# Optimization experiments

Measured on AMD Instinct MI355X. Metric: run time of the kernel, lower is better.

Reference implementation:

```python
import jax, jax.numpy as jnp
import numpy as np

T, B = 1024, 512
IN_F, HID, OUT = 64, 128, 2
DT = 0.001

# SuperSpike surrogate gradient (norse default threshold method='super')
@jax.custom_vjp
def superspike(x, alpha):
    return (x > 0).astype(x.dtype)

def _ss_fwd(x, alpha):
    return superspike(x, alpha), (x, alpha)

def _ss_bwd(res, g):
    x, alpha = res
    return (g / (alpha * jnp.abs(x) + 1.0) ** 2, jnp.zeros_like(alpha))

superspike.defvjp(_ss_fwd, _ss_bwd)


def setup_inputs() -> dict:
    key = jax.random.key(0)
    ks = jax.random.split(key, 6)
    x = jax.random.normal(ks[0], (T, B, IN_F), jnp.float32)
    # nn.Linear(input, hidden, bias=False)
    W_in = jax.random.normal(ks[1], (HID, IN_F), jnp.float32) / np.sqrt(IN_F)
    # LIFRecurrentCell(hidden, hidden) weights (norse init scale sqrt(2/hidden))
    cell_W_in = jax.random.normal(ks[2], (HID, HID), jnp.float32) * np.sqrt(2.0 / HID)
    cell_W_rec = jax.random.normal(ks[3], (HID, HID), jnp.float32) * np.sqrt(2.0 / HID)
    cell_W_rec = cell_W_rec * (1.0 - jnp.eye(HID, dtype=jnp.float32))  # autapses=False
    # nn.Linear(hidden, output, bias=True)
    W_out = jax.random.normal(ks[4], (OUT, HID), jnp.float32) / np.sqrt(HID)
    b_out = jax.random.normal(ks[5], (OUT,), jnp.float32) * 0.01
    # LIFParameters as in __init__
    alpha = jnp.full((HID,), 100.0, jnp.float32)
    v_th = jnp.full((HID,), 1.0, jnp.float32)
    v_leak = jnp.asarray(0.0, jnp.float32)
    v_reset = jnp.full((HID,), 0.0, jnp.float32)
    tau_mem_inv = jnp.full((HID,), 100.0, jnp.float32)
    tau_syn_inv = jnp.full((HID,), 200.0, jnp.float32)
    return dict(x=x, W_in=W_in, cell_W_in=cell_W_in, cell_W_rec=cell_W_rec,
                W_out=W_out, b_out=b_out, alpha=alpha, v_th=v_th, v_leak=v_leak,
                v_reset=v_reset, tau_mem_inv=tau_mem_inv, tau_syn_inv=tau_syn_inv)


def reference(x, W_in, cell_W_in, cell_W_rec, W_out, b_out,
              alpha, v_th, v_leak, v_reset, tau_mem_inv, tau_syn_inv):
    Tn, Bn, _ = x.shape
    H = W_in.shape[0]

    def step(carry, x_t):
        z, v, i = carry                                   # each [B,H]
        inp = x_t @ W_in.T                                # input_layer
        # norse _lif_step: decay v and i, spike, reset, inject currents
        v_dec = v + DT * tau_mem_inv * ((v_leak - v) + i)
        i_dec = i - DT * tau_syn_inv * i
        z_new = superspike(v_dec - v_th, alpha)
        v_new = (1.0 - z_new) * v_dec + z_new * v_reset
        i_new = i_dec + inp @ cell_W_in.T + z @ cell_W_rec.T
        out_t = z_new @ W_out.T + b_out                   # output_layer
        return (z_new, v_new, i_new), (out_t, jnp.sum(z_new))

    init = (jnp.zeros((Bn, H), x.dtype),
            jnp.zeros((Bn, H), x.dtype),
            jnp.zeros((Bn, H), x.dtype))
    _, (outs, spk) = jax.lax.scan(step, init, x)
    z_sum = jnp.sum(outs, axis=0)                         # __decode_sum over time
    spikerate = jnp.sum(spk) / (Tn * Bn * H)
    return z_sum, spikerate
```

## Files before the change

kernel.cpp:

```cpp
#include <hip/hip_runtime.h>
#include <stdint.h>

#define T_STEPS 1024
#define BATCH   512
#define INF     64
#define HID     128
#define OUTF    2

__global__ void zero_kernel(unsigned int* __restrict__ counter)
{
    *counter = 0u;
}

#define FOR16(M) M(0)M(1)M(2)M(3)M(4)M(5)M(6)M(7)M(8)M(9)M(10)M(11)M(12)M(13)M(14)M(15)
#define FOR32(M) FOR16(M) M(16)M(17)M(18)M(19)M(20)M(21)M(22)M(23)M(24)M(25)M(26)M(27)M(28)M(29)M(30)M(31)

#define BARRIER() asm volatile("s_waitcnt lgkmcnt(0)\n\ts_barrier" ::: "memory")

__global__ __launch_bounds__(256) __attribute__((amdgpu_waves_per_eu(2, 2)))
void snn_seq(const float* __restrict__ x,
             const float* __restrict__ W_in,
             const float* __restrict__ cWi,
             const float* __restrict__ Wrec,
             const float* __restrict__ W_out,
             const float* __restrict__ b_out,
             const float* __restrict__ v_th,
             const float* __restrict__ v_leak1,
             const float* __restrict__ v_reset,
             const float* __restrict__ tau_mem,
             const float* __restrict__ tau_syn,
             float* __restrict__ out,
             unsigned int* __restrict__ counter)
{
    #pragma clang fp contract(off)

    extern __shared__ char smem[];
    float* Wrec_T  = (float*)smem;
    float* x_lds   = Wrec_T + HID * HID;
    float* inp_lds = x_lds + 2 * INF;
    float* pre_lds = inp_lds + 2 * HID;

    const int tid = threadIdx.x;
    const int b   = blockIdx.x;

    for (int idx = tid; idx < HID * HID; idx += 256)
        Wrec_T[idx] = Wrec[(idx & (HID - 1)) * HID + (idx >> 7)];
    if (tid >= 128 && tid < 192) {
        int l = tid - 128;
        x_lds[0 * INF + l] = x[(size_t)(0 * BATCH + b) * INF + l];
        x_lds[1 * INF + l] = x[(size_t)(1 * BATCH + b) * INF + l];
    }
    __syncthreads();

    if (tid < 128) {
        const int h = tid;
        const float4* cwr = (const float4*)(cWi + h * HID);
        #define DECL_C(q) float4 c##q = cwr[q];
        FOR32(DECL_C)
        #undef DECL_C

        BARRIER();

        {
            const float4* ir4 = (const float4*)(inp_lds + 0 * HID);
            float p = 0.f;
            #define S2(q) { float4 i4 = ir4[q]; \
                p = fmaf(i4.x, c##q.x, p); p = fmaf(i4.y, c##q.y, p); \
                p = fmaf(i4.z, c##q.z, p); p = fmaf(i4.w, c##q.w, p); }
            FOR32(S2)
            pre_lds[0 * HID + h] = p;
            BARRIER();

            for (int i = 0; i < T_STEPS; ++i) {
                const int nbuf = (i & 1) ^ 1;
                const float4* ir = (const float4*)(inp_lds + nbuf * HID);
                float pp = 0.f;
                #undef S2
                #define S2(q) { float4 i4 = ir[q]; \
                    pp = fmaf(i4.x, c##q.x, pp); pp = fmaf(i4.y, c##q.y, pp); \
                    pp = fmaf(i4.z, c##q.z, pp); pp = fmaf(i4.w, c##q.w, pp); }
                FOR32(S2)
                #undef S2
                pre_lds[nbuf * HID + h] = pp;
                BARRIER();
            }
        }
    } else if (tid < 192) {
        const int l = tid - 128;
        const float4* wra = (const float4*)(W_in + l * INF);
        const float4* wrb = (const float4*)(W_in + (l + 64) * INF);
        #define DECL_AB(q) float4 a##q = wra[q]; float4 b##q = wrb[q];
        FOR16(DECL_AB)
        #undef DECL_AB

        #define S1(q) { float4 x4 = xr4[q]; \
            sa = fmaf(x4.x, a##q.x, sa); sa = fmaf(x4.y, a##q.y, sa); \
            sa = fmaf(x4.z, a##q.z, sa); sa = fmaf(x4.w, a##q.w, sa); \
            sb = fmaf(x4.x, b##q.x, sb); sb = fmaf(x4.y, b##q.y, sb); \
            sb = fmaf(x4.z, b##q.z, sb); sb = fmaf(x4.w, b##q.w, sb); }

        {
            const float4* xr4 = (const float4*)(x_lds + 0 * INF);
            float sa = 0.f, sb = 0.f;
            FOR16(S1)
            inp_lds[0 * HID + l] = sa;
            inp_lds[0 * HID + 64 + l] = sb;
        }
        BARRIER();

        float xnext;
        {
            const float4* xr4 = (const float4*)(x_lds + 1 * INF);
            float sa = 0.f, sb = 0.f;
            FOR16(S1)
            inp_lds[1 * HID + l] = sa;
            inp_lds[1 * HID + 64 + l] = sb;
            x_lds[0 * INF + l] = x[(size_t)(2 * BATCH + b) * INF + l];
            xnext = x[(size_t)(3 * BATCH + b) * INF + l];
        }
        BARRIER();

        for (int i = 0; i < T_STEPS; ++i) {
            const int buf  = i & 1;
            const int nbuf = buf ^ 1;
            x_lds[nbuf * INF + l] = xnext;
            int tn = (i + 4 < T_STEPS) ? i + 4 : T_STEPS - 1;
            xnext = x[((size_t)tn * BATCH + b) * INF + l];
            const float4* xr4 = (const float4*)(x_lds + buf * INF);
            float sa = 0.f, sb = 0.f;
            FOR16(S1)
            inp_lds[buf * HID + l] = sa;
            inp_lds[buf * HID + 64 + l] = sb;
            BARRIER();
        }
        #undef S1
    } else {
        const int l  = tid - 192;
        const int h0 = 2 * l, h1 = 2 * l + 1;

        const double vth0  = (double)v_th[h0],    vth1  = (double)v_th[h1];
        const double vleak = (double)v_leak1[0];
        const double vrs0  = (double)v_reset[h0], vrs1  = (double)v_reset[h1];
        const double dtm0  = 0.001 * (double)tau_mem[h0];
        const double dtm1  = 0.001 * (double)tau_mem[h1];
        const double dts0  = 0.001 * (double)tau_syn[h0];
        const double dts1  = 0.001 * (double)tau_syn[h1];

        double v0 = 0.0, v1 = 0.0, c0 = 0.0, c1 = 0.0;
        int cnt0 = 0, cnt1 = 0;
        unsigned long long me = 0ull, mo = 0ull;

        BARRIER();
        BARRIER();

        for (int i = 0; i < T_STEPS; ++i) {
            const int buf = i & 1;
            float2 pp = *(const float2*)(pre_lds + buf * HID + h0);

            double s00 = 0.0, s01 = 0.0, s10 = 0.0, s11 = 0.0;
            {
                unsigned long long A = me, Bm = mo;
                while (A | Bm) {
                    float2 w0 = make_float2(0.f, 0.f), w1 = w0, w2 = w0, w3 = w0,
                           w4 = w0, w5 = w0, w6 = w0, w7 = w0;
                    if (A)  { int j = __builtin_ctzll(A);  A  &= A - 1;  w0 = *(const float2*)(Wrec_T + (2 * j) * HID + h0); }
                    if (A)  { int j = __builtin_ctzll(A);  A  &= A - 1;  w1 = *(const float2*)(Wrec_T + (2 * j) * HID + h0); }
                    if (A)  { int j = __builtin_ctzll(A);  A  &= A - 1;  w2 = *(const float2*)(Wrec_T + (2 * j) * HID + h0); }
                    if (A)  { int j = __builtin_ctzll(A);  A  &= A - 1;  w3 = *(const float2*)(Wrec_T + (2 * j) * HID + h0); }
                    if (Bm) { int j = __builtin_ctzll(Bm); Bm &= Bm - 1; w4 = *(const float2*)(Wrec_T + (2 * j + 1) * HID + h0); }
                    if (Bm) { int j = __builtin_ctzll(Bm); Bm &= Bm - 1; w5 = *(const float2*)(Wrec_T + (2 * j + 1) * HID + h0); }
                    if (Bm) { int j = __builtin_ctzll(Bm); Bm &= Bm - 1; w6 = *(const float2*)(Wrec_T + (2 * j + 1) * HID + h0); }
                    if (Bm) { int j = __builtin_ctzll(Bm); Bm &= Bm - 1; w7 = *(const float2*)(Wrec_T + (2 * j + 1) * HID + h0); }
                    s00 += (double)w0.x; s10 += (double)w0.y;
                    s01 += (double)w1.x; s11 += (double)w1.y;
                    s00 += (double)w2.x; s10 += (double)w2.y;
                    s01 += (double)w3.x; s11 += (double)w3.y;
                    s00 += (double)w4.x; s10 += (double)w4.y;
                    s01 += (double)w5.x; s11 += (double)w5.y;
                    s00 += (double)w6.x; s10 += (double)w6.y;
                    s01 += (double)w7.x; s11 += (double)w7.y;
                }
            }
            double rec0 = s00 + s01;
            double rec1 = s10 + s11;

            double vd0 = v0 + dtm0 * ((vleak - v0) + c0);
            double id0 = c0 - dts0 * c0;
            bool   z0  = (vd0 - vth0) > 0.0;
            v0 = z0 ? vrs0 : vd0;
            c0 = (id0 + (double)pp.x) + rec0;
            cnt0 += z0 ? 1 : 0;

            double vd1 = v1 + dtm1 * ((vleak - v1) + c1);
            double id1 = c1 - dts1 * c1;
            bool   z1  = (vd1 - vth1) > 0.0;
            v1 = z1 ? vrs1 : vd1;
            c1 = (id1 + (double)pp.y) + rec1;
            cnt1 += z1 ? 1 : 0;

            me = __ballot(z0);
            mo = __ballot(z1);
            BARRIER();
        }

        pre_lds[h0] = (float)cnt0;
        pre_lds[h1] = (float)cnt1;
    }

    __syncthreads();

    const float* cnt_lds = pre_lds;
    if (tid < OUTF) {
        double sAcc = 0.0;
        for (int hh = 0; hh < HID; ++hh)
            sAcc += (double)cnt_lds[hh] * (double)W_out[tid * HID + hh];
        out[(size_t)b * OUTF + tid] = (float)(sAcc + 1024.0 * (double)b_out[tid]);
    }
    if (tid == 0) {
        unsigned int tot = 0;
        for (int k2 = 0; k2 < HID; ++k2) tot += (unsigned int)cnt_lds[k2];
        atomicAdd(counter, tot);
    }
}

__global__ void finalize_kernel(float* __restrict__ out)
{
    unsigned int c = ((const unsigned int*)out)[BATCH * OUTF];
    out[BATCH * OUTF] = (float)c * 0x1p-26f;
}

extern "C" void kernel_launch(void* const* d_in, const int* in_sizes, int n_in,
                              void* d_out, int out_size, void* d_ws, size_t ws_size,
                              hipStream_t stream) {
    (void)in_sizes; (void)n_in; (void)d_ws; (void)ws_size; (void)out_size;

    const float* x       = (const float*)d_in[0];
    const float* W_in    = (const float*)d_in[1];
    const float* cWi     = (const float*)d_in[2];
    const float* cWr     = (const float*)d_in[3];
    const float* W_out   = (const float*)d_in[4];
    const float* b_out   = (const float*)d_in[5];
    const float* v_th    = (const float*)d_in[7];
    const float* v_leak  = (const float*)d_in[8];
    const float* v_reset = (const float*)d_in[9];
    const float* tau_mem = (const float*)d_in[10];
    const float* tau_syn = (const float*)d_in[11];
    float* out = (float*)d_out;
    unsigned int* counter = (unsigned int*)out + BATCH * OUTF;

    zero_kernel<<<1, 1, 0, stream>>>(counter);

    const size_t lds_bytes =
        (size_t)(HID * HID + 2 * INF + 2 * HID + 2 * HID) * sizeof(float);
    snn_seq<<<dim3(512), dim3(256), lds_bytes, stream>>>(
        x, W_in, cWi, cWr, W_out, b_out, v_th, v_leak, v_reset,
        tau_mem, tau_syn, out, counter);

    finalize_kernel<<<1, 1, 0, stream>>>(out);
}
```

Before: 733.6 us.

## Deepen warp-specialized pipeline to 8 waves with split matvec stages

Doubles the block to 512 threads and splits the per-step work into more pipeline stages. The cell input matvec is split across two wavefronts that each hold half the weights. The input projection now uses 128 threads, each computing one output. A dedicated wavefront prefetches x into a 4-slot ring. The aim is to shorten each stage's critical path so the barrier-synchronised step loop runs faster, at the cost of more waves, more barriers in flight and extra pipeline latency.

```diff
diff --git a/kernel.cpp b/kernel.cpp
--- a/kernel.cpp
+++ b/kernel.cpp
@@ -13,11 +13,9 @@
 }
 
 #define FOR16(M) M(0)M(1)M(2)M(3)M(4)M(5)M(6)M(7)M(8)M(9)M(10)M(11)M(12)M(13)M(14)M(15)
-#define FOR32(M) FOR16(M) M(16)M(17)M(18)M(19)M(20)M(21)M(22)M(23)M(24)M(25)M(26)M(27)M(28)M(29)M(30)M(31)
-
 #define BARRIER() asm volatile("s_waitcnt lgkmcnt(0)\n\ts_barrier" ::: "memory")
 
-__global__ __launch_bounds__(256) __attribute__((amdgpu_waves_per_eu(2, 2)))
+__global__ __launch_bounds__(512, 4)
 void snn_seq(const float* __restrict__ x,
              const float* __restrict__ W_in,
              const float* __restrict__ cWi,
@@ -36,106 +34,144 @@
 
     extern __shared__ char smem[];
     float* Wrec_T  = (float*)smem;
-    float* x_lds   = Wrec_T + HID * HID;
-    float* inp_lds = x_lds + 2 * INF;
-    float* pre_lds = inp_lds + 2 * HID;
+    float* inp_lds = Wrec_T + HID * HID;
+    float* x_lds   = inp_lds + 4 * HID;
+    float* q_lds   = x_lds + 4 * INF;
+    float* pre_lds = q_lds + 2 * HID;
 
     const int tid = threadIdx.x;
     const int b   = blockIdx.x;
 
-    for (int idx = tid; idx < HID * HID; idx += 256)
+    for (int idx = tid; idx < HID * HID; idx += 512)
         Wrec_T[idx] = Wrec[(idx & (HID - 1)) * HID + (idx >> 7)];
-    if (tid >= 128 && tid < 192) {
-        int l = tid - 128;
-        x_lds[0 * INF + l] = x[(size_t)(0 * BATCH + b) * INF + l];
-        x_lds[1 * INF + l] = x[(size_t)(1 * BATCH + b) * INF + l];
-    }
-    __syncthreads();
 
     if (tid < 128) {
         const int h = tid;
         const float4* cwr = (const float4*)(cWi + h * HID);
         #define DECL_C(q) float4 c##q = cwr[q];
-        FOR32(DECL_C)
+        FOR16(DECL_C)
         #undef DECL_C
 
-        BARRIER();
-
+        #define S2A(q) { float4 i4 = ir4[q]; \
+            acc = fmaf(i4.x, c##q.x, acc); acc = fmaf(i4.y, c##q.y, acc); \
+            acc = fmaf(i4.z, c##q.z, acc); acc = fmaf(i4.w, c##q.w, acc); }
+
+        __syncthreads();
+        BARRIER();
         {
             const float4* ir4 = (const float4*)(inp_lds + 0 * HID);
-            float p = 0.f;
-            #define S2(q) { float4 i4 = ir4[q]; \
-                p = fmaf(i4.x, c##q.x, p); p = fmaf(i4.y, c##q.y, p); \
-                p = fmaf(i4.z, c##q.z, p); p = fmaf(i4.w, c##q.w, p); }
-            FOR32(S2)
-            pre_lds[0 * HID + h] = p;
-            BARRIER();
-
-            for (int i = 0; i < T_STEPS; ++i) {
-                const int nbuf = (i & 1) ^ 1;
-                const float4* ir = (const float4*)(inp_lds + nbuf * HID);
-                float pp = 0.f;
-                #undef S2
-                #define S2(q) { float4 i4 = ir[q]; \
-                    pp = fmaf(i4.x, c##q.x, pp); pp = fmaf(i4.y, c##q.y, pp); \
-                    pp = fmaf(i4.z, c##q.z, pp); pp = fmaf(i4.w, c##q.w, pp); }
-                FOR32(S2)
-                #undef S2
-                pre_lds[nbuf * HID + h] = pp;
-                BARRIER();
-            }
-        }
-    } else if (tid < 192) {
-        const int l = tid - 128;
+            float acc = 0.f; FOR16(S2A)
+            q_lds[0 * HID + h] = acc;
+        }
+        BARRIER();
+        {
+            const float4* ir4 = (const float4*)(inp_lds + 1 * HID);
+            float acc = 0.f; FOR16(S2A)
+            q_lds[1 * HID + h] = acc;
+        }
+        BARRIER();
+        for (int i = 0; i < T_STEPS; i += 2) {
+            {
+                const float4* ir4 = (const float4*)(inp_lds + ((i + 2) & 3) * HID);
+                float acc = 0.f; FOR16(S2A)
+                q_lds[0 * HID + h] = acc;
+            }
+            BARRIER();
+            {
+                const float4* ir4 = (const float4*)(inp_lds + ((i + 3) & 3) * HID);
+                float acc = 0.f; FOR16(S2A)
+                q_lds[1 * HID + h] = acc;
+            }
+            BARRIER();
+        }
+        #undef S2A
+    } else if (tid < 256) {
+        const int h = tid - 128;
+        const float4* cwr = (const float4*)(cWi + h * HID) + 16;
+        #define DECL_D(q) float4 d##q = cwr[q];
+        FOR16(DECL_D)
+        #undef DECL_D
+
+        #define S2B(q) { float4 i4 = ir4[q]; \
+            acc = fmaf(i4.x, d##q.x, acc); acc = fmaf(i4.y, d##q.y, acc); \
+            acc = fmaf(i4.z, d##q.z, acc); acc = fmaf(i4.w, d##q.w, acc); }
+
+        __syncthreads();
+        BARRIER();
+        BARRIER();
+        {
+            const float4* ir4 = (const float4*)(inp_lds + 0 * HID) + 16;
+            float acc = q_lds[0 * HID + h];
+            FOR16(S2B)
+            pre_lds[0 * HID + h] = acc;
+        }
+        BARRIER();
+        for (int i = 0; i < T_STEPS; i += 2) {
+            {
+                const float4* ir4 = (const float4*)(inp_lds + ((i + 1) & 3) * HID) + 16;
+                float acc = q_lds[1 * HID + h];
+                FOR16(S2B)
+                pre_lds[1 * HID + h] = acc;
+            }
+            BARRIER();
+            {
+                const float4* ir4 = (const float4*)(inp_lds + ((i + 2) & 3) * HID) + 16;
+                float acc = q_lds[0 * HID + h];
+                FOR16(S2B)
+                pre_lds[0 * HID + h] = acc;
+            }
+            BARRIER();
+        }
+        #undef S2B
+    } else if (tid < 384) {
+        const int l = tid - 256;
         const float4* wra = (const float4*)(W_in + l * INF);
-        const float4* wrb = (const float4*)(W_in + (l + 64) * INF);
-        #define DECL_AB(q) float4 a##q = wra[q]; float4 b##q = wrb[q];
-        FOR16(DECL_AB)
-        #undef DECL_AB
+        #define DECL_A(q) float4 a##q = wra[q];
+        FOR16(DECL_A)
+        #undef DECL_A
 
         #define S1(q) { float4 x4 = xr4[q]; \
-            sa = fmaf(x4.x, a##q.x, sa); sa = fmaf(x4.y, a##q.y, sa); \
-            sa = fmaf(x4.z, a##q.z, sa); sa = fmaf(x4.w, a##q.w, sa); \
-            sb = fmaf(x4.x, b##q.x, sb); sb = fmaf(x4.y, b##q.y, sb); \
-            sb = fmaf(x4.z, b##q.z, sb); sb = fmaf(x4.w, b##q.w, sb); }
-
+            acc = fmaf(x4.x, a##q.x, acc); acc = fmaf(x4.y, a##q.y, acc); \
+            acc = fmaf(x4.z, a##q.z, acc); acc = fmaf(x4.w, a##q.w, acc); }
+
+        __syncthreads();
         {
             const float4* xr4 = (const float4*)(x_lds + 0 * INF);
-            float sa = 0.f, sb = 0.f;
-            FOR16(S1)
-            inp_lds[0 * HID + l] = sa;
-            inp_lds[0 * HID + 64 + l] = sb;
-        }
-        BARRIER();
-
-        float xnext;
+            float acc = 0.f; FOR16(S1)
+            inp_lds[0 * HID + l] = acc;
+        }
+        BARRIER();
         {
             const float4* xr4 = (const float4*)(x_lds + 1 * INF);
-            float sa = 0.f, sb = 0.f;
-            FOR16(S1)
-            inp_lds[1 * HID + l] = sa;
-            inp_lds[1 * HID + 64 + l] = sb;
-            x_lds[0 * INF + l] = x[(size_t)(2 * BATCH + b) * INF + l];
-            xnext = x[(size_t)(3 * BATCH + b) * INF + l];
-        }
-        BARRIER();
-
-        for (int i = 0; i < T_STEPS; ++i) {
-            const int buf  = i & 1;
-            const int nbuf = buf ^ 1;
-            x_lds[nbuf * INF + l] = xnext;
-            int tn = (i + 4 < T_STEPS) ? i + 4 : T_STEPS - 1;
-            xnext = x[((size_t)tn * BATCH + b) * INF + l];
-            const float4* xr4 = (const float4*)(x_lds + buf * INF);
-            float sa = 0.f, sb = 0.f;
-            FOR16(S1)
-            inp_lds[buf * HID + l] = sa;
-            inp_lds[buf * HID + 64 + l] = sb;
+            float acc = 0.f; FOR16(S1)
+            inp_lds[1 * HID + l] = acc;
+        }
+        BARRIER();
+        {
+            const float4* xr4 = (const float4*)(x_lds + 2 * INF);
+            float acc = 0.f; FOR16(S1)
+            inp_lds[2 * HID + l] = acc;
+        }
+        BARRIER();
+        for (int i = 0; i < T_STEPS; i += 2) {
+            {
+                const int s = (i + 3) & 3;
+                const float4* xr4 = (const float4*)(x_lds + s * INF);
+                float acc = 0.f; FOR16(S1)
+                inp_lds[s * HID + l] = acc;
+            }
+            BARRIER();
+            {
+                const int s = (i + 4) & 3;
+                const float4* xr4 = (const float4*)(x_lds + s * INF);
+                float acc = 0.f; FOR16(S1)
+                inp_lds[s * HID + l] = acc;
+            }
             BARRIER();
         }
         #undef S1
-    } else {
-        const int l  = tid - 192;
+    } else if (tid < 448) {
+        const int l  = tid - 384;
         const int h0 = 2 * l, h1 = 2 * l + 1;
 
         const double vth0  = (double)v_th[h0],    vth1  = (double)v_th[h1];
@@ -150,12 +186,11 @@
         int cnt0 = 0, cnt1 = 0;
         unsigned long long me = 0ull, mo = 0ull;
 
-        BARRIER();
-        BARRIER();
+        __syncthreads();
+        BARRIER(); BARRIER(); BARRIER();
 
         for (int i = 0; i < T_STEPS; ++i) {
-            const int buf = i & 1;
-            float2 pp = *(const float2*)(pre_lds + buf * HID + h0);
+            float2 pp = *(const float2*)(pre_lds + (i & 1) * HID + h0);
 
             double s00 = 0.0, s01 = 0.0, s10 = 0.0, s11 = 0.0;
             {
@@ -205,6 +240,39 @@
 
         pre_lds[h0] = (float)cnt0;
         pre_lds[h1] = (float)cnt1;
+    } else {
+        const int l = tid - 448;
+        float t0 = x[(size_t)(0 * BATCH + b) * INF + l];
+        float t1 = x[(size_t)(1 * BATCH + b) * INF + l];
+        float t2 = x[(size_t)(2 * BATCH + b) * INF + l];
+        float t3 = x[(size_t)(3 * BATCH + b) * INF + l];
+        x_lds[0 * INF + l] = t0;
+        x_lds[1 * INF + l] = t1;
+        x_lds[2 * INF + l] = t2;
+        x_lds[3 * INF + l] = t3;
+        float rC = x[(size_t)(4 * BATCH + b) * INF + l];
+        float rA = x[(size_t)(5 * BATCH + b) * INF + l];
+        float rB = x[(size_t)(6 * BATCH + b) * INF + l];
+
+        __syncthreads();
+        BARRIER();
+        BARRIER();
+        x_lds[0 * INF + l] = rC;
+        BARRIER();
+        for (int i = 0; i < T_STEPS; i += 2) {
+            {
+                x_lds[((i + 5) & 3) * INF + l] = rA;
+                int tn = (i + 7 < T_STEPS) ? i + 7 : T_STEPS - 1;
+                rA = x[((size_t)tn * BATCH + b) * INF + l];
+            }
+            BARRIER();
+            {
+                x_lds[((i + 6) & 3) * INF + l] = rB;
+                int tn = (i + 8 < T_STEPS) ? i + 8 : T_STEPS - 1;
+                rB = x[((size_t)tn * BATCH + b) * INF + l];
+            }
+            BARRIER();
+        }
     }
 
     __syncthreads();
@@ -251,8 +319,8 @@
     zero_kernel<<<1, 1, 0, stream>>>(counter);
 
     const size_t lds_bytes =
-        (size_t)(HID * HID + 2 * INF + 2 * HID + 2 * HID) * sizeof(float);
-    snn_seq<<<dim3(512), dim3(256), lds_bytes, stream>>>(
+        (size_t)(HID * HID + 4 * HID + 4 * INF + 2 * HID + 2 * HID) * sizeof(float);
+    snn_seq<<<dim3(512), dim3(512), lds_bytes, stream>>>(
         x, W_in, cWi, cWr, W_out, b_out, v_th, v_leak, v_reset,
         tau_mem, tau_syn, out, counter);
 
```

Measured after the change: 617.3 us. 1.19x faster.

## Split per-step matvecs into deeper multi-wave pipeline across 14 waves per block

Applied to the files above, without the earlier changes.

The kernel grows from 256 to 896 threads per block. The input projection and the cWi projection are split across multiple waves along K, chained through LDS partial sums with staggered time offsets, which makes a software pipeline several steps deep. A dedicated wave now prefetches x into a 4-deep ring, and the spike-driven recurrent gather unrolls 16 instead of 8. The aim is to shorten the per-step critical path of the serial recurrence, at the cost of more warmup steps and more barrier participants per step.

```diff
diff --git a/kernel.cpp b/kernel.cpp
--- a/kernel.cpp
+++ b/kernel.cpp
@@ -7,17 +7,28 @@
 #define HID     128
 #define OUTF    2
 
+typedef float f32x4 __attribute__((ext_vector_type(4)));
+
 __global__ void zero_kernel(unsigned int* __restrict__ counter)
 {
     *counter = 0u;
 }
 
-#define FOR16(M) M(0)M(1)M(2)M(3)M(4)M(5)M(6)M(7)M(8)M(9)M(10)M(11)M(12)M(13)M(14)M(15)
-#define FOR32(M) FOR16(M) M(16)M(17)M(18)M(19)M(20)M(21)M(22)M(23)M(24)M(25)M(26)M(27)M(28)M(29)M(30)M(31)
-
 #define BARRIER() asm volatile("s_waitcnt lgkmcnt(0)\n\ts_barrier" ::: "memory")
 
-__global__ __launch_bounds__(256) __attribute__((amdgpu_waves_per_eu(2, 2)))
+#define GLD0(d,p)  asm volatile("global_load_dwordx4 %0, %1, off"            : "=v"(d) : "v"(p) : "memory")
+#define GLD(d,p,o) asm volatile("global_load_dwordx4 %0, %1, off offset:" #o : "=v"(d) : "v"(p) : "memory")
+#define VMWAIT()   asm volatile("s_waitcnt vmcnt(0)" ::: "memory")
+#define LOAD8(p) \
+    GLD0(w0,(p)); GLD(w1,(p),16); GLD(w2,(p),32); GLD(w3,(p),48); \
+    GLD(w4,(p),64); GLD(w5,(p),80); GLD(w6,(p),96); GLD(w7,(p),112); VMWAIT()
+
+#define CH(q) { float4 i4 = ir[q]; \
+    acc = fmaf(i4.x, w##q.x, acc); acc = fmaf(i4.y, w##q.y, acc); \
+    acc = fmaf(i4.z, w##q.z, acc); acc = fmaf(i4.w, w##q.w, acc); }
+#define CH8 CH(0)CH(1)CH(2)CH(3)CH(4)CH(5)CH(6)CH(7)
+
+__global__ __launch_bounds__(896, 7)
 void snn_seq(const float* __restrict__ x,
              const float* __restrict__ W_in,
              const float* __restrict__ cWi,
@@ -36,106 +47,62 @@
 
     extern __shared__ char smem[];
     float* Wrec_T  = (float*)smem;
-    float* x_lds   = Wrec_T + HID * HID;
-    float* inp_lds = x_lds + 2 * INF;
-    float* pre_lds = inp_lds + 2 * HID;
+    float* inp_lds = Wrec_T + HID * HID;
+    float* x_lds   = inp_lds + 8 * HID;
+    float* p1_lds  = x_lds + 4 * INF;
+    float* p2_lds  = p1_lds + 2 * HID;
+    float* p3_lds  = p2_lds + 2 * HID;
+    float* r1_lds  = p3_lds + 2 * HID;
+    float* pre_lds = r1_lds + 2 * HID;
 
     const int tid = threadIdx.x;
     const int b   = blockIdx.x;
 
-    for (int idx = tid; idx < HID * HID; idx += 256)
+    for (int idx = tid; idx < HID * HID; idx += 896)
         Wrec_T[idx] = Wrec[(idx & (HID - 1)) * HID + (idx >> 7)];
-    if (tid >= 128 && tid < 192) {
-        int l = tid - 128;
-        x_lds[0 * INF + l] = x[(size_t)(0 * BATCH + b) * INF + l];
-        x_lds[1 * INF + l] = x[(size_t)(1 * BATCH + b) * INF + l];
-    }
-    __syncthreads();
-
-    if (tid < 128) {
-        const int h = tid;
-        const float4* cwr = (const float4*)(cWi + h * HID);
-        #define DECL_C(q) float4 c##q = cwr[q];
-        FOR32(DECL_C)
-        #undef DECL_C
-
-        BARRIER();
-
-        {
-            const float4* ir4 = (const float4*)(inp_lds + 0 * HID);
-            float p = 0.f;
-            #define S2(q) { float4 i4 = ir4[q]; \
-                p = fmaf(i4.x, c##q.x, p); p = fmaf(i4.y, c##q.y, p); \
-                p = fmaf(i4.z, c##q.z, p); p = fmaf(i4.w, c##q.w, p); }
-            FOR32(S2)
-            pre_lds[0 * HID + h] = p;
-            BARRIER();
-
-            for (int i = 0; i < T_STEPS; ++i) {
-                const int nbuf = (i & 1) ^ 1;
-                const float4* ir = (const float4*)(inp_lds + nbuf * HID);
-                float pp = 0.f;
-                #undef S2
-                #define S2(q) { float4 i4 = ir[q]; \
-                    pp = fmaf(i4.x, c##q.x, pp); pp = fmaf(i4.y, c##q.y, pp); \
-                    pp = fmaf(i4.z, c##q.z, pp); pp = fmaf(i4.w, c##q.w, pp); }
-                FOR32(S2)
-                #undef S2
-                pre_lds[nbuf * HID + h] = pp;
-                BARRIER();
-            }
-        }
-    } else if (tid < 192) {
-        const int l = tid - 128;
-        const float4* wra = (const float4*)(W_in + l * INF);
-        const float4* wrb = (const float4*)(W_in + (l + 64) * INF);
-        #define DECL_AB(q) float4 a##q = wra[q]; float4 b##q = wrb[q];
-        FOR16(DECL_AB)
-        #undef DECL_AB
-
-        #define S1(q) { float4 x4 = xr4[q]; \
-            sa = fmaf(x4.x, a##q.x, sa); sa = fmaf(x4.y, a##q.y, sa); \
-            sa = fmaf(x4.z, a##q.z, sa); sa = fmaf(x4.w, a##q.w, sa); \
-            sb = fmaf(x4.x, b##q.x, sb); sb = fmaf(x4.y, b##q.y, sb); \
-            sb = fmaf(x4.z, b##q.z, sb); sb = fmaf(x4.w, b##q.w, sb); }
-
-        {
-            const float4* xr4 = (const float4*)(x_lds + 0 * INF);
-            float sa = 0.f, sb = 0.f;
-            FOR16(S1)
-            inp_lds[0 * HID + l] = sa;
-            inp_lds[0 * HID + 64 + l] = sb;
-        }
-        BARRIER();
-
-        float xnext;
-        {
-            const float4* xr4 = (const float4*)(x_lds + 1 * INF);
-            float sa = 0.f, sb = 0.f;
-            FOR16(S1)
-            inp_lds[1 * HID + l] = sa;
-            inp_lds[1 * HID + 64 + l] = sb;
-            x_lds[0 * INF + l] = x[(size_t)(2 * BATCH + b) * INF + l];
-            xnext = x[(size_t)(3 * BATCH + b) * INF + l];
-        }
-        BARRIER();
-
-        for (int i = 0; i < T_STEPS; ++i) {
-            const int buf  = i & 1;
-            const int nbuf = buf ^ 1;
-            x_lds[nbuf * INF + l] = xnext;
-            int tn = (i + 4 < T_STEPS) ? i + 4 : T_STEPS - 1;
-            xnext = x[((size_t)tn * BATCH + b) * INF + l];
-            const float4* xr4 = (const float4*)(x_lds + buf * INF);
-            float sa = 0.f, sb = 0.f;
-            FOR16(S1)
-            inp_lds[buf * HID + l] = sa;
-            inp_lds[buf * HID + 64 + l] = sb;
-            BARRIER();
-        }
-        #undef S1
-    } else {
-        const int l  = tid - 192;
+
+    if (tid < 512) {
+        const int h    = tid & (HID - 1);
+        const int st   = tid >> 7;
+        const int koff = st * 32;
+        f32x4 w0, w1, w2, w3, w4, w5, w6, w7;
+        LOAD8(cWi + h * HID + koff);
+        float* inP  = (st == 1) ? p1_lds : (st == 2) ? p2_lds : p3_lds;
+        float* outP = (st == 0) ? p1_lds : (st == 1) ? p2_lds
+                    : (st == 2) ? p3_lds : pre_lds;
+        const int toff = 4 - st;
+        BARRIER();
+        for (int i = -6; i < T_STEPS; ++i) {
+            const int t = i + toff;
+            if (t >= 0 && t < T_STEPS) {
+                const float4* ir = (const float4*)(inp_lds + (t & 7) * HID + koff);
+                float acc = (st == 0) ? 0.f : inP[(t & 1) * HID + h];
+                CH8
+                outP[(t & 1) * HID + h] = acc;
+            }
+            BARRIER();
+        }
+    } else if (tid < 768) {
+        const int h    = tid & (HID - 1);
+        const int sub  = (tid - 512) >> 7;
+        const int koff = sub * 32;
+        f32x4 w0, w1, w2, w3, w4, w5, w6, w7;
+        LOAD8(W_in + h * INF + koff);
+        const int toff = 6 - sub;
+        BARRIER();
+        for (int i = -6; i < T_STEPS; ++i) {
+            const int t = i + toff;
+            if (t >= 0 && t < T_STEPS) {
+                const float4* ir = (const float4*)(x_lds + (t & 3) * INF + koff);
+                float acc = (sub == 0) ? 0.f : r1_lds[(t & 1) * HID + h];
+                CH8
+                if (sub == 0) r1_lds[(t & 1) * HID + h] = acc;
+                else          inp_lds[(t & 7) * HID + h] = acc;
+            }
+            BARRIER();
+        }
+    } else if (tid < 832) {
+        const int l  = tid - 768;
         const int h0 = 2 * l, h1 = 2 * l + 1;
 
         const double vth0  = (double)v_th[h0],    vth1  = (double)v_th[h1];
@@ -151,60 +118,95 @@
         unsigned long long me = 0ull, mo = 0ull;
 
         BARRIER();
-        BARRIER();
-
-        for (int i = 0; i < T_STEPS; ++i) {
-            const int buf = i & 1;
-            float2 pp = *(const float2*)(pre_lds + buf * HID + h0);
-
-            double s00 = 0.0, s01 = 0.0, s10 = 0.0, s11 = 0.0;
-            {
-                unsigned long long A = me, Bm = mo;
-                while (A | Bm) {
-                    float2 w0 = make_float2(0.f, 0.f), w1 = w0, w2 = w0, w3 = w0,
-                           w4 = w0, w5 = w0, w6 = w0, w7 = w0;
-                    if (A)  { int j = __builtin_ctzll(A);  A  &= A - 1;  w0 = *(const float2*)(Wrec_T + (2 * j) * HID + h0); }
-                    if (A)  { int j = __builtin_ctzll(A);  A  &= A - 1;  w1 = *(const float2*)(Wrec_T + (2 * j) * HID + h0); }
-                    if (A)  { int j = __builtin_ctzll(A);  A  &= A - 1;  w2 = *(const float2*)(Wrec_T + (2 * j) * HID + h0); }
-                    if (A)  { int j = __builtin_ctzll(A);  A  &= A - 1;  w3 = *(const float2*)(Wrec_T + (2 * j) * HID + h0); }
-                    if (Bm) { int j = __builtin_ctzll(Bm); Bm &= Bm - 1; w4 = *(const float2*)(Wrec_T + (2 * j + 1) * HID + h0); }
-                    if (Bm) { int j = __builtin_ctzll(Bm); Bm &= Bm - 1; w5 = *(const float2*)(Wrec_T + (2 * j + 1) * HID + h0); }
-                    if (Bm) { int j = __builtin_ctzll(Bm); Bm &= Bm - 1; w6 = *(const float2*)(Wrec_T + (2 * j + 1) * HID + h0); }
-                    if (Bm) { int j = __builtin_ctzll(Bm); Bm &= Bm - 1; w7 = *(const float2*)(Wrec_T + (2 * j + 1) * HID + h0); }
-                    s00 += (double)w0.x; s10 += (double)w0.y;
-                    s01 += (double)w1.x; s11 += (double)w1.y;
-                    s00 += (double)w2.x; s10 += (double)w2.y;
-                    s01 += (double)w3.x; s11 += (double)w3.y;
-                    s00 += (double)w4.x; s10 += (double)w4.y;
-                    s01 += (double)w5.x; s11 += (double)w5.y;
-                    s00 += (double)w6.x; s10 += (double)w6.y;
-                    s01 += (double)w7.x; s11 += (double)w7.y;
+        for (int i = -6; i < T_STEPS; ++i) {
+            if (i >= 0) {
+                float2 pp = *(const float2*)(pre_lds + (i & 1) * HID + h0);
+
+                double q00 = 0.0, q01 = 0.0, q10 = 0.0, q11 = 0.0;
+                {
+                    unsigned long long A = me, B = mo;
+                    while (A | B) {
+                        float2 wv0 = make_float2(0.f, 0.f), wv1 = wv0, wv2 = wv0, wv3 = wv0,
+                               wv4 = wv0, wv5 = wv0, wv6 = wv0, wv7 = wv0,
+                               wv8 = wv0, wv9 = wv0, wva = wv0, wvb = wv0,
+                               wvc = wv0, wvd = wv0, wve = wv0, wvf = wv0;
+                        if (A) { int j = __builtin_ctzll(A); A &= A - 1; wv0 = *(const float2*)(Wrec_T + (2 * j) * HID + h0); }
+                        if (A) { int j = __builtin_ctzll(A); A &= A - 1; wv1 = *(const float2*)(Wrec_T + (2 * j) * HID + h0); }
+                        if (A) { int j = __builtin_ctzll(A); A &= A - 1; wv2 = *(const float2*)(Wrec_T + (2 * j) * HID + h0); }
+                        if (A) { int j = __builtin_ctzll(A); A &= A - 1; wv3 = *(const float2*)(Wrec_T + (2 * j) * HID + h0); }
+                        if (A) { int j = __builtin_ctzll(A); A &= A - 1; wv4 = *(const float2*)(Wrec_T + (2 * j) * HID + h0); }
+                        if (A) { int j = __builtin_ctzll(A); A &= A - 1; wv5 = *(const float2*)(Wrec_T + (2 * j) * HID + h0); }
+                        if (A) { int j = __builtin_ctzll(A); A &= A - 1; wv6 = *(const float2*)(Wrec_T + (2 * j) * HID + h0); }
+                        if (A) { int j = __builtin_ctzll(A); A &= A - 1; wv7 = *(const float2*)(Wrec_T + (2 * j) * HID + h0); }
+                        if (B) { int j = __builtin_ctzll(B); B &= B - 1; wv8 = *(const float2*)(Wrec_T + (2 * j + 1) * HID + h0); }
+                        if (B) { int j = __builtin_ctzll(B); B &= B - 1; wv9 = *(const float2*)(Wrec_T + (2 * j + 1) * HID + h0); }
+                        if (B) { int j = __builtin_ctzll(B); B &= B - 1; wva = *(const float2*)(Wrec_T + (2 * j + 1) * HID + h0); }
+                        if (B) { int j = __builtin_ctzll(B); B &= B - 1; wvb = *(const float2*)(Wrec_T + (2 * j + 1) * HID + h0); }
+                        if (B) { int j = __builtin_ctzll(B); B &= B - 1; wvc = *(const float2*)(Wrec_T + (2 * j + 1) * HID + h0); }
+                        if (B) { int j = __builtin_ctzll(B); B &= B - 1; wvd = *(const float2*)(Wrec_T + (2 * j + 1) * HID + h0); }
+                        if (B) { int j = __builtin_ctzll(B); B &= B - 1; wve = *(const float2*)(Wrec_T + (2 * j + 1) * HID + h0); }
+                        if (B) { int j = __builtin_ctzll(B); B &= B - 1; wvf = *(const float2*)(Wrec_T + (2 * j + 1) * HID + h0); }
+                        q00 += (double)wv0.x; q10 += (double)wv0.y;
+                        q01 += (double)wv1.x; q11 += (double)wv1.y;
+                        q00 += (double)wv2.x; q10 += (double)wv2.y;
+                        q01 += (double)wv3.x; q11 += (double)wv3.y;
+                        q00 += (double)wv4.x; q10 += (double)wv4.y;
+                        q01 += (double)wv5.x; q11 += (double)wv5.y;
+                        q00 += (double)wv6.x; q10 += (double)wv6.y;
+                        q01 += (double)wv7.x; q11 += (double)wv7.y;
+                        q00 += (double)wv8.x; q10 += (double)wv8.y;
+                        q01 += (double)wv9.x; q11 += (double)wv9.y;
+                        q00 += (double)wva.x; q10 += (double)wva.y;
+                        q01 += (double)wvb.x; q11 += (double)wvb.y;
+                        q00 += (double)wvc.x; q10 += (double)wvc.y;
+                        q01 += (double)wvd.x; q11 += (double)wvd.y;
+                        q00 += (double)wve.x; q10 += (double)wve.y;
+                        q01 += (double)wvf.x; q11 += (double)wvf.y;
+                    }
                 }
-            }
-            double rec0 = s00 + s01;
-            double rec1 = s10 + s11;
-
-            double vd0 = v0 + dtm0 * ((vleak - v0) + c0);
-            double id0 = c0 - dts0 * c0;
-            bool   z0  = (vd0 - vth0) > 0.0;
-            v0 = z0 ? vrs0 : vd0;
-            c0 = (id0 + (double)pp.x) + rec0;
-            cnt0 += z0 ? 1 : 0;
-
-            double vd1 = v1 + dtm1 * ((vleak - v1) + c1);
-            double id1 = c1 - dts1 * c1;
-            bool   z1  = (vd1 - vth1) > 0.0;
-            v1 = z1 ? vrs1 : vd1;
-            c1 = (id1 + (double)pp.y) + rec1;
-            cnt1 += z1 ? 1 : 0;
-
-            me = __ballot(z0);
-            mo = __ballot(z1);
-            BARRIER();
-        }
-
+                double rec0 = q00 + q01;
+                double rec1 = q10 + q11;
+
+                double vd0 = v0 + dtm0 * ((vleak - v0) + c0);
+                double id0 = c0 - dts0 * c0;
+                bool   z0  = (vd0 - vth0) > 0.0;
+                v0 = z0 ? vrs0 : vd0;
+                c0 = (id0 + (double)pp.x) + rec0;
+                cnt0 += z0 ? 1 : 0;
+
+                double vd1 = v1 + dtm1 * ((vleak - v1) + c1);
+                double id1 = c1 - dts1 * c1;
+                bool   z1  = (vd1 - vth1) > 0.0;
+                v1 = z1 ? vrs1 : vd1;
+                c1 = (id1 + (double)pp.y) + rec1;
+                cnt1 += z1 ? 1 : 0;
+
+                me = __ballot(z0);
+                mo = __ballot(z1);
+            }
+            BARRIER();
+        }
         pre_lds[h0] = (float)cnt0;
         pre_lds[h1] = (float)cnt1;
+    } else {
+        const int l = tid - 832;
+        x_lds[0 * INF + l] = x[(size_t)(0 * BATCH + b) * INF + l];
+        x_lds[1 * INF + l] = x[(size_t)(1 * BATCH + b) * INF + l];
+        x_lds[2 * INF + l] = x[(size_t)(2 * BATCH + b) * INF + l];
+        x_lds[3 * INF + l] = x[(size_t)(3 * BATCH + b) * INF + l];
+        float rA = x[(size_t)(4 * BATCH + b) * INF + l];
+        float rB = x[(size_t)(5 * BATCH + b) * INF + l];
+        BARRIER();
+        for (int i = -6; i < T_STEPS; ++i) {
+            const int t = i + 7;
+            if (t >= 4 && t < T_STEPS) {
+                x_lds[(t & 3) * INF + l] = rA;
+                rA = rB;
+                int tn = (t + 2 < T_STEPS) ? t + 2 : T_STEPS - 1;
+                rB = x[((size_t)tn * BATCH + b) * INF + l];
+            }
+            BARRIER();
+        }
     }
 
     __syncthreads();
@@ -251,8 +253,8 @@
     zero_kernel<<<1, 1, 0, stream>>>(counter);
 
     const size_t lds_bytes =
-        (size_t)(HID * HID + 2 * INF + 2 * HID + 2 * HID) * sizeof(float);
-    snn_seq<<<dim3(512), dim3(256), lds_bytes, stream>>>(
+        (size_t)(HID * HID + 8 * HID + 4 * INF + 5 * 2 * HID) * sizeof(float);
+    snn_seq<<<dim3(512), dim3(896), lds_bytes, stream>>>(
         x, W_in, cWi, cWr, W_out, b_out, v_th, v_leak, v_reset,
         tau_mem, tau_syn, out, counter);
 
```

Result: slower. 2.547 ms (+247.1%).
